# Performance work log

Hardware: AMD Instinct MI355X
Metric: run time of the kernel (lower is better)

## Reference

```python
import jax, jax.numpy as jnp
import numpy as np

B, S, D, H = 4, 1024, 768, 12
DH = D // H            # 64
MAXPOS = 1024          # config.max_position_embeddings
NTYPES = 8             # flow types (embedding has NTYPES+1 rows, row 0 = padding)


def setup_inputs() -> dict:
    key = jax.random.key(0)
    ks = jax.random.split(key, 12)
    sc = 0.02
    inp = {
        "hidden_states": jax.random.normal(ks[0], (B, S, D), jnp.float32),
        "Wq": jax.random.normal(ks[1], (D, D), jnp.float32) * sc,
        "bq": jnp.zeros((D,), jnp.float32),
        "Wk": jax.random.normal(ks[2], (D, D), jnp.float32) * sc,
        "bk": jnp.zeros((D,), jnp.float32),
        "Wv": jax.random.normal(ks[3], (D, D), jnp.float32) * sc,
        "bv": jnp.zeros((D,), jnp.float32),
        "dist_emb": jax.random.normal(ks[4], (2 * MAXPOS - 1, DH), jnp.float32) * sc,
        "cfg_emb": jax.random.normal(ks[5], (NTYPES + 1, 1), jnp.float32) * sc,
        "dfg_emb": jax.random.normal(ks[6], (NTYPES + 1, 1), jnp.float32) * sc,
        "rfg_emb": jax.random.normal(ks[7], (NTYPES + 1, 1), jnp.float32) * sc,
        "cfg_matrix": jax.random.randint(ks[8], (B, S, S), 0, NTYPES + 1, jnp.int32),
        "dfg_matrix": jax.random.randint(ks[9], (B, S, S), 0, NTYPES + 1, jnp.int32),
        "rdg_matrix": jax.random.randint(ks[10], (B, S, S), 0, NTYPES + 1, jnp.int32),
    }
    return inp


def reference(hidden_states, Wq, bq, Wk, bk, Wv, bv, dist_emb,
              cfg_emb, dfg_emb, rfg_emb, cfg_matrix, dfg_matrix, rdg_matrix):
    b, s, d = hidden_states.shape
    inv_sqrt = 1.0 / float(np.sqrt(DH))

    def heads(x):  # [b,s,d] -> [b,H,s,DH]
        return x.reshape(b, s, H, DH).transpose(0, 2, 1, 3)

    q = heads(hidden_states @ Wq.T + bq)
    k = heads(hidden_states @ Wk.T + bk)
    v = heads(hidden_states @ Wv.T + bv)

    scores = jnp.einsum('bhld,bhrd->bhlr', q, k)

    # relative_key_query positional bias
    dist = jnp.arange(s)[:, None] - jnp.arange(s)[None, :] + (MAXPOS - 1)
    pe = dist_emb[dist]  # [s, s, DH]
    scores = scores + jnp.einsum('bhld,lrd->bhlr', q, pe) \
                    + jnp.einsum('bhrd,lrd->bhlr', k, pe)

    scores = scores * inv_sqrt

    # flow-type bias: scalar embedding per (i,j), padding row 0 forced to zero
    flow = (cfg_emb.at[0].set(0.0)[cfg_matrix][..., 0]
            + dfg_emb.at[0].set(0.0)[dfg_matrix][..., 0]
            + rfg_emb.at[0].set(0.0)[rdg_matrix][..., 0])  # [b,s,s]
    scores = scores + flow[:, None, :, :]

    probs = jax.nn.softmax(scores, axis=-1)
    ctx = jnp.einsum('bhlr,bhrd->bhld', probs, v)
    return ctx.transpose(0, 2, 1, 3).reshape(b, s, d)
```

## Files before the change

### kernel.cpp

```cpp
#include <hip/hip_runtime.h>


typedef __attribute__((ext_vector_type(4))) float f32x4;
typedef __attribute__((ext_vector_type(8))) short s16x8;

#define MFMA_BF16 __builtin_amdgcn_mfma_f32_16x16x32_bf16

__device__ __forceinline__ unsigned short f2bf(float x) {
  unsigned u = __builtin_bit_cast(unsigned, x);
  u += 0x7fffu + ((u >> 16) & 1u);
  return (unsigned short)(u >> 16);
}
__device__ __forceinline__ float bf2f(unsigned short h) {
  unsigned u = ((unsigned)h) << 16;
  return __builtin_bit_cast(float, u);
}
__device__ __forceinline__ float exp2_fast(float x) {
  float r;
  asm("v_exp_f32 %0, %1" : "=v"(r) : "v"(x));
  return r;
}
__device__ __forceinline__ void gl_lds16(const void* g, void* l) {
  __builtin_amdgcn_global_load_lds(
      (const __attribute__((address_space(1))) unsigned int*)g,
      (__attribute__((address_space(3))) unsigned int*)l, 16, 0, 0);
}

__global__ __launch_bounds__(256) void k_prep(
    const float* __restrict__ hs, const float* __restrict__ wq,
    const float* __restrict__ wk, const float* __restrict__ wv,
    const float* __restrict__ de, unsigned short* __restrict__ hsb,
    unsigned short* __restrict__ wb, unsigned short* __restrict__ db) {
  const long HSN = 3145728, WN = 1769472;
  long e = ((long)blockIdx.x * 256 + threadIdx.x) * 4;
  if (e < HSN) {
    float4 v = *(const float4*)(hs + e);
    *(ushort4*)(hsb + e) = make_ushort4(f2bf(v.x), f2bf(v.y), f2bf(v.z), f2bf(v.w));
  } else if (e < HSN + WN) {
    long ew = e - HSN;
    const float* src = (ew >= 1179648) ? wv : ((ew >= 589824) ? wk : wq);
    long off = (ew >= 1179648) ? (ew - 1179648) : ((ew >= 589824) ? (ew - 589824) : ew);
    float4 v = *(const float4*)(src + off);
    *(ushort4*)(wb + ew) = make_ushort4(f2bf(v.x), f2bf(v.y), f2bf(v.z), f2bf(v.w));
  } else {
    long ed = e - HSN - WN;
    ushort4 ov;
    if (ed < 131008) {
      float4 v = *(const float4*)(de + ed);
      ov = make_ushort4(f2bf(v.x), f2bf(v.y), f2bf(v.z), f2bf(v.w));
    } else {
      ov = make_ushort4(0, 0, 0, 0);
    }
    *(ushort4*)(db + ed) = ov;
  }
}

__global__ __launch_bounds__(256) void k_flow(
    const int* __restrict__ cm, const int* __restrict__ dm,
    const int* __restrict__ rm, const float* __restrict__ ce,
    const float* __restrict__ dfe, const float* __restrict__ rfe,
    unsigned short* __restrict__ flT) {
  const int tid = threadIdx.x;
  const int rt = blockIdx.x, lt = blockIdx.y, b = blockIdx.z;
  const int l15 = tid & 15, g = (tid >> 4) & 3, w = tid >> 6;
  const int rowb = lt * 64 + w * 16 + g * 4;
  const int colb = rt * 64 + l15;
  s16x8 o0, o1;
#pragma unroll
  for (int n = 0; n < 4; ++n) {
#pragma unroll
    for (int r = 0; r < 4; ++r) {
      const long idx = ((long)b << 20) + ((long)(rowb + r) << 10) + colb + (n << 4);
      const int c = cm[idx], d = dm[idx], rr = rm[idx];
      const float v = (c ? ce[c] : 0.f) + (d ? dfe[d] : 0.f) + (rr ? rfe[rr] : 0.f);
      const short hv = (short)f2bf(1.4426950408889634f * v);
      if (n < 2) o0[n * 4 + r] = hv; else o1[(n - 2) * 4 + r] = hv;
    }
  }
  unsigned short* dst =
      flT + ((long)((((b << 4) + lt) << 4) | rt) << 12) + (tid << 4);
  *(s16x8*)(dst) = o0;
  *(s16x8*)(dst + 8) = o1;
}

__global__ __launch_bounds__(256) void k_qkv(
    const unsigned short* __restrict__ A, const unsigned short* __restrict__ W,
    const float* __restrict__ bq, const float* __restrict__ bk,
    const float* __restrict__ bv, unsigned short* __restrict__ Qp,
    unsigned short* __restrict__ Kp, unsigned short* __restrict__ Vp) {
  __shared__ __align__(16) char smq[16384];
  char* sa = smq;
  char* sb = smq + 8192;
  const int tid = threadIdx.x, w = tid >> 6, lane = tid & 63;
  const int g = lane >> 4, l15 = lane & 15;
  const int n0 = blockIdx.x * 128, m0 = blockIdx.y * 128;
  const int wm = w >> 1, wn = w & 1;
  f32x4 acc[4][4] = {};
  for (int k0 = 0; k0 < 768; k0 += 32) {
#pragma unroll
    for (int it = 0; it < 2; ++it) {
      const int c = (w << 7) + (it << 6) + lane;
      const int row = c >> 2, sl = c & 3;
      const int so = ((sl ^ ((row >> 1) & 3)) << 3);
      char* dst = smq + ((w << 7) + (it << 6)) * 16;
      gl_lds16(A + (long)(m0 + row) * 768 + k0 + so, dst);
      gl_lds16(W + (long)(n0 + row) * 768 + k0 + so, dst + 8192);
    }
    __syncthreads();
    s16x8 af[4], bf[4];
#pragma unroll
    for (int mi = 0; mi < 4; ++mi) {
      const int row = wm * 64 + mi * 16 + l15;
      af[mi] = *(const s16x8*)(sa + row * 64 + ((g ^ ((row >> 1) & 3)) << 4));
    }
#pragma unroll
    for (int ni = 0; ni < 4; ++ni) {
      const int row = wn * 64 + ni * 16 + l15;
      bf[ni] = *(const s16x8*)(sb + row * 64 + ((g ^ ((row >> 1) & 3)) << 4));
    }
#pragma unroll
    for (int mi = 0; mi < 4; ++mi)
#pragma unroll
      for (int ni = 0; ni < 4; ++ni)
        acc[mi][ni] = MFMA_BF16(af[mi], bf[ni], acc[mi][ni], 0, 0, 0);
    __syncthreads();
  }
  const int t_sel = n0 / 768;
  const float* bias = (t_sel == 0) ? bq : (t_sel == 1) ? bk : bv;
  unsigned short* dst = (t_sel == 0) ? Qp : (t_sel == 1) ? Kp : Vp;
#pragma unroll
  for (int ni = 0; ni < 4; ++ni) {
    const int mcol = n0 + wn * 64 + ni * 16 + l15;
    const int nw2 = mcol - t_sel * 768;
    const float bvv = bias[nw2];
    const int h = nw2 >> 6, dh = nw2 & 63;
#pragma unroll
    for (int mi = 0; mi < 4; ++mi) {
#pragma unroll
      for (int r = 0; r < 4; ++r) {
        const int token = m0 + wm * 64 + mi * 16 + (g << 2) + r;
        const int b = token >> 10, s = token & 1023;
        const long idx = ((((long)(b * 12 + h)) << 10) + s) * 64 + dh;
        dst[idx] = f2bf(acc[mi][ni][r] + bvv);
      }
    }
  }
}

__global__ __launch_bounds__(256) void k_vt(const unsigned short* __restrict__ Vp,
                                            unsigned short* __restrict__ Vt) {
  __shared__ __align__(16) unsigned short t[64][64];
  const int bh = blockIdx.y, s0 = blockIdx.x * 64;
  const int tid = threadIdx.x;
#pragma unroll
  for (int it = 0; it < 2; ++it) {
    const int c = it * 256 + tid;
    const int row = c >> 3, sl = c & 7;
    const int slot = sl ^ ((row >> 3) & 7);
    s16x8 v = *(const s16x8*)(Vp + (((long)bh << 10) + s0 + row) * 64 + sl * 8);
    *(s16x8*)&t[row][slot * 8] = v;
  }
  __syncthreads();
#pragma unroll
  for (int it = 0; it < 2; ++it) {
    const int c = it * 256 + tid;
    const int d = c >> 3, ss = c & 7;
    const int cg = d >> 3;
    s16x8 vv;
#pragma unroll
    for (int i = 0; i < 8; ++i) {
      const int rr = ss * 8 + i;
      vv[i] = (short)t[rr][((cg ^ ((rr >> 3) & 7)) << 3) + (d & 7)];
    }
    *(s16x8*)(Vt + (((long)bh * 64 + d) << 10) + s0 + ss * 8) = vv;
  }
}

__global__ __launch_bounds__(256, 3) void k_attn(
    const unsigned short* __restrict__ Qp, const unsigned short* __restrict__ Kp,
    const unsigned short* __restrict__ Vtp, const unsigned short* __restrict__ Db,
    const unsigned short* __restrict__ FlT, float* __restrict__ Out) {
  __shared__ __align__(16) char sm[50688];
  char* Kl = sm;
  char* Vl = sm + 8192;
  char* Dl = sm + 16384;
  unsigned short* QDs = (unsigned short*)(sm + 32768);
  char* Pl = sm + 32768;
  unsigned short* KDs = (unsigned short*)(sm + 41984);

  const int tid = threadIdx.x, w = tid >> 6, lane = tid & 63;
  const int g = lane >> 4, l15 = lane & 15;
  const int l0 = blockIdx.x << 6, h = blockIdx.y, b = blockIdx.z;
  const int bh = b * 12 + h;
  const unsigned short* Qb = Qp + ((long)bh << 16);
  const unsigned short* Kb = Kp + ((long)bh << 16);
  const unsigned short* Vb = Vtp + ((long)bh << 16);
  const unsigned short* fTb =
      FlT + ((long)(((b << 4) + blockIdx.x) << 4) << 12) + (tid << 4);

  const int qrow = l0 + (w << 4) + l15;
  const s16x8 qf0 = *(const s16x8*)(Qb + (long)qrow * 64 + g * 8);
  const s16x8 qf1 = *(const s16x8*)(Qb + (long)qrow * 64 + 32 + g * 8);

  f32x4 oacc[4] = {};
  float lpart[4] = {0.f, 0.f, 0.f, 0.f};

  for (int rt = 0; rt < 16; ++rt) {
    const int r0 = rt << 6;
    const int t0 = l0 - r0 + 960;

    const s16x8 fv0 = *(const s16x8*)(fTb + ((long)rt << 12));
    const s16x8 fv1 = *(const s16x8*)(fTb + ((long)rt << 12) + 8);

#pragma unroll
    for (int it = 0; it < 2; ++it) {
      const int c = (w << 7) + (it << 6) + lane;
      const int row = c >> 3, sl = c & 7;
      const int so = ((sl ^ (row & 7)) << 3);
      char* dst = sm + ((w << 7) + (it << 6)) * 16;
      gl_lds16(Kb + (long)(r0 + row) * 64 + so, dst);
      gl_lds16(Vb + (long)row * 1024 + r0 + so, dst + 8192);
    }
    {
      const int nh = (rt == 0) ? 2 : 1;
      for (int hh = 0; hh < nh; ++hh) {
        const int ts = t0 + (hh << 6);
        char* dhalf = Dl + (((ts >> 6) & 1) << 13);
#pragma unroll
        for (int it = 0; it < 2; ++it) {
          const int c = (w << 7) + (it << 6) + lane;
          const int row = c >> 3, sl = c & 7;
          gl_lds16(Db + (long)(ts + row) * 64 + ((sl ^ (row & 7)) << 3),
                   dhalf + ((w << 7) + (it << 6)) * 16);
        }
      }
    }
    __syncthreads();

    {
      const int krow = (w << 4) + l15;
      const s16x8 kf0 = *(const s16x8*)(Kl + krow * 128 + ((g ^ (krow & 7)) << 4));
      const s16x8 kf1 = *(const s16x8*)(Kl + krow * 128 + (((4 + g) ^ (krow & 7)) << 4));
#pragma unroll
      for (int n = 0; n < 8; ++n) {
        const bool doQ = (n >= w) && (n <= w + 4);
        const bool doK = (n >= 3 - w) && (n <= 7 - w);
        if (!(doQ || doK)) continue;
        const int pb = ((((t0 >> 6) + (n >> 2)) & 1) << 6) + ((n & 3) << 4);
        const int trow = pb + l15;
        const s16x8 d0 = *(const s16x8*)(Dl + trow * 128 + ((g ^ (trow & 7)) << 4));
        const s16x8 d1 = *(const s16x8*)(Dl + trow * 128 + (((4 + g) ^ (trow & 7)) << 4));
        f32x4 qa = {}, ka = {};
        if (doQ) {
          qa = MFMA_BF16(qf0, d0, qa, 0, 0, 0);
          qa = MFMA_BF16(qf1, d1, qa, 0, 0, 0);
        }
        if (doK) {
          ka = MFMA_BF16(kf0, d0, ka, 0, 0, 0);
          ka = MFMA_BF16(kf1, d1, ka, 0, 0, 0);
        }
#pragma unroll
        for (int r = 0; r < 4; ++r) {
          const int prow = (w << 4) + (g << 2) + r;
          const int u = (n << 4) + l15;
          if (doQ) {
            const int cq = u - prow;
            if ((unsigned)cq < 64u) QDs[prow * 72 + cq] = f2bf(qa[r]);
          }
          if (doK) {
            const int ck = u + prow - 63;
            if ((unsigned)ck < 64u) KDs[prow * 68 + ck] = f2bf(ka[r]);
          }
        }
      }
    }
    __syncthreads();

    f32x4 sacc[4] = {};
#pragma unroll
    for (int n = 0; n < 4; ++n) {
      const int kr = (n << 4) + l15;
      const s16x8 b0 = *(const s16x8*)(Kl + kr * 128 + ((g ^ (kr & 7)) << 4));
      const s16x8 b1 = *(const s16x8*)(Kl + kr * 128 + (((4 + g) ^ (kr & 7)) << 4));
      sacc[n] = MFMA_BF16(qf0, b0, sacc[n], 0, 0, 0);
      sacc[n] = MFMA_BF16(qf1, b1, sacc[n], 0, 0, 0);
    }
#pragma unroll
    for (int n = 0; n < 4; ++n) {
#pragma unroll
      for (int r = 0; r < 4; ++r) {
        const int ib = (w << 4) + (g << 2) + r;
        const int j = (n << 4) + l15;
        const float qd = bf2f(QDs[ib * 72 + (63 - j)]);
        const float kd = bf2f(KDs[j * 68 + ib]);
        const float fv = bf2f((unsigned short)(
            n < 2 ? fv0[(n << 2) + r] : fv1[((n - 2) << 2) + r]));
        sacc[n][r] = (sacc[n][r] + qd + kd) * 0.18033688f + fv;
      }
    }

#pragma unroll
    for (int r = 0; r < 4; ++r) {
      const float p0 = exp2_fast(sacc[0][r]);
      const float p1 = exp2_fast(sacc[1][r]);
      const float p2 = exp2_fast(sacc[2][r]);
      const float p3 = exp2_fast(sacc[3][r]);
      sacc[0][r] = p0; sacc[1][r] = p1; sacc[2][r] = p2; sacc[3][r] = p3;
      lpart[r] += (p0 + p1) + (p2 + p3);
    }

#pragma unroll
    for (int n = 0; n < 4; ++n) {
#pragma unroll
      for (int r = 0; r < 4; ++r) {
        const int ib = (w << 4) + (g << 2) + r;
        const int j = (n << 4) + l15;
        *(unsigned short*)(Pl + ib * 144 + (((j >> 3) ^ (ib & 7)) << 4) +
                           ((j & 7) << 1)) = f2bf(sacc[n][r]);
      }
    }

#pragma unroll
    for (int k0 = 0; k0 < 2; ++k0) {
      const int prow = (w << 4) + l15;
      const s16x8 pf = *(const s16x8*)(
          Pl + prow * 144 + ((((k0 << 2) + g) ^ (prow & 7)) << 4));
#pragma unroll
      for (int n = 0; n < 4; ++n) {
        const int vrow = (n << 4) + l15;
        const s16x8 vf = *(const s16x8*)(
            Vl + vrow * 128 + ((((k0 << 2) + g) ^ (vrow & 7)) << 4));
        oacc[n] = MFMA_BF16(pf, vf, oacc[n], 0, 0, 0);
      }
    }
    __syncthreads();
  }

  float lsum[4];
#pragma unroll
  for (int r = 0; r < 4; ++r) {
    float s = lpart[r];
#pragma unroll
    for (int dd = 1; dd < 16; dd <<= 1) s += __shfl_xor(s, dd, 64);
    lsum[r] = s;
  }
#pragma unroll
  for (int n = 0; n < 4; ++n) {
#pragma unroll
    for (int r = 0; r < 4; ++r) {
      const int l = l0 + (w << 4) + (g << 2) + r;
      const int d = (n << 4) + l15;
      Out[((long)(b * 1024 + l)) * 768 + h * 64 + d] = oacc[n][r] / lsum[r];
    }
  }
}

extern "C" void kernel_launch(void* const* d_in, const int* in_sizes, int n_in,
                              void* d_out, int out_size, void* d_ws, size_t ws_size,
                              hipStream_t stream) {
  const float* hs = (const float*)d_in[0];
  const float* Wq = (const float*)d_in[1];
  const float* bq = (const float*)d_in[2];
  const float* Wk = (const float*)d_in[3];
  const float* bk = (const float*)d_in[4];
  const float* Wv = (const float*)d_in[5];
  const float* bv = (const float*)d_in[6];
  const float* de = (const float*)d_in[7];
  const float* ce = (const float*)d_in[8];
  const float* dfe = (const float*)d_in[9];
  const float* rfe = (const float*)d_in[10];
  const int* cm = (const int*)d_in[11];
  const int* dm = (const int*)d_in[12];
  const int* rm = (const int*)d_in[13];
  float* out = (float*)d_out;
  char* ws = (char*)d_ws;

  unsigned short* hsb = (unsigned short*)(ws + 0);
  unsigned short* wb  = (unsigned short*)(ws + 6291456);
  unsigned short* db  = (unsigned short*)(ws + 9830400);
  unsigned short* flT = (unsigned short*)(ws + 10092544);
  unsigned short* qp  = (unsigned short*)(ws + 18481152);
  unsigned short* kp  = (unsigned short*)(ws + 24772608);
  unsigned short* vp  = (unsigned short*)(ws + 31064064);
  unsigned short* vt  = (unsigned short*)(ws + 37355520);

  k_prep<<<4928, 256, 0, stream>>>(hs, Wq, Wk, Wv, de, hsb, wb, db);
  k_flow<<<dim3(16, 16, 4), 256, 0, stream>>>(cm, dm, rm, ce, dfe, rfe, flT);
  k_qkv<<<dim3(18, 32), 256, 0, stream>>>(hsb, wb, bq, bk, bv, qp, kp, vp);
  k_vt<<<dim3(16, 48), 256, 0, stream>>>(vp, vt);
  k_attn<<<dim3(16, 12, 4), 256, 0, stream>>>(qp, kp, vt, db, flT, out);
}
```

Baseline: 137.7 us.

## Keep Q-side relative-position bias in registers via ds_bpermute instead of LDS

The Q·dist_emb bias tiles are now computed into a register array of five MFMA accumulators per wave. The diagonal shift is done with lane permutes (ds_bpermute using precomputed source addresses and masks) rather than a round trip through the QDs shared buffer. The K-side bias loop is also made branch-free over its exact five tiles, with bounds checks only on the edge tiles. This removes LDS stores and loads and the bf16 rounding on the Q path, at the cost of more registers and permute instructions.

```diff
diff --git a/kernel.cpp b/kernel.cpp
--- a/kernel.cpp
+++ b/kernel.cpp
@@ -184,9 +184,8 @@
   char* Kl = sm;
   char* Vl = sm + 8192;
   char* Dl = sm + 16384;
-  unsigned short* QDs = (unsigned short*)(sm + 32768);
-  char* Pl = sm + 32768;
-  unsigned short* KDs = (unsigned short*)(sm + 41984);
+  unsigned short* KDs = (unsigned short*)(sm + 32768);
+  char* Pl = sm + 41472;
 
   const int tid = threadIdx.x, w = tid >> 6, lane = tid & 63;
   const int g = lane >> 4, l15 = lane & 15;
@@ -202,6 +201,16 @@
   const s16x8 qf0 = *(const s16x8*)(Qb + (long)qrow * 64 + g * 8);
   const s16x8 qf1 = *(const s16x8*)(Qb + (long)qrow * 64 + 32 + g * 8);
 
+  int srcad[4];
+  bool msk[4];
+#pragma unroll
+  for (int r = 0; r < 4; ++r) {
+    const int bl = ((g << 2) + r - 1) & 15;
+    srcad[r] = (((lane & 48) + ((bl - l15) & 15)) << 2);
+    msk[r] = (l15 <= bl);
+  }
+  const bool g0 = (g == 0);
+
   f32x4 oacc[4] = {};
   float lpart[4] = {0.f, 0.f, 0.f, 0.f};
 
@@ -237,39 +246,42 @@
     }
     __syncthreads();
 
+    f32x4 qa[5];
+#pragma unroll
+    for (int lt = 0; lt < 5; ++lt) {
+      const int nq = w + lt;
+      const int pb = ((((t0 >> 6) + (nq >> 2)) & 1) << 6) + ((nq & 3) << 4);
+      const int trow = pb + l15;
+      const s16x8 d0 = *(const s16x8*)(Dl + trow * 128 + ((g ^ (trow & 7)) << 4));
+      const s16x8 d1 = *(const s16x8*)(Dl + trow * 128 + (((4 + g) ^ (trow & 7)) << 4));
+      f32x4 a = {};
+      a = MFMA_BF16(qf0, d0, a, 0, 0, 0);
+      a = MFMA_BF16(qf1, d1, a, 0, 0, 0);
+      qa[lt] = a;
+    }
+
     {
       const int krow = (w << 4) + l15;
       const s16x8 kf0 = *(const s16x8*)(Kl + krow * 128 + ((g ^ (krow & 7)) << 4));
       const s16x8 kf1 = *(const s16x8*)(Kl + krow * 128 + (((4 + g) ^ (krow & 7)) << 4));
 #pragma unroll
-      for (int n = 0; n < 8; ++n) {
-        const bool doQ = (n >= w) && (n <= w + 4);
-        const bool doK = (n >= 3 - w) && (n <= 7 - w);
-        if (!(doQ || doK)) continue;
-        const int pb = ((((t0 >> 6) + (n >> 2)) & 1) << 6) + ((n & 3) << 4);
+      for (int kt = 0; kt < 5; ++kt) {
+        const int nk = 3 - w + kt;
+        const int pb = ((((t0 >> 6) + (nk >> 2)) & 1) << 6) + ((nk & 3) << 4);
         const int trow = pb + l15;
         const s16x8 d0 = *(const s16x8*)(Dl + trow * 128 + ((g ^ (trow & 7)) << 4));
         const s16x8 d1 = *(const s16x8*)(Dl + trow * 128 + (((4 + g) ^ (trow & 7)) << 4));
-        f32x4 qa = {}, ka = {};
-        if (doQ) {
-          qa = MFMA_BF16(qf0, d0, qa, 0, 0, 0);
-          qa = MFMA_BF16(qf1, d1, qa, 0, 0, 0);
-        }
-        if (doK) {
-          ka = MFMA_BF16(kf0, d0, ka, 0, 0, 0);
-          ka = MFMA_BF16(kf1, d1, ka, 0, 0, 0);
-        }
+        f32x4 ka = {};
+        ka = MFMA_BF16(kf0, d0, ka, 0, 0, 0);
+        ka = MFMA_BF16(kf1, d1, ka, 0, 0, 0);
 #pragma unroll
         for (int r = 0; r < 4; ++r) {
           const int prow = (w << 4) + (g << 2) + r;
-          const int u = (n << 4) + l15;
-          if (doQ) {
-            const int cq = u - prow;
-            if ((unsigned)cq < 64u) QDs[prow * 72 + cq] = f2bf(qa[r]);
-          }
-          if (doK) {
-            const int ck = u + prow - 63;
+          const int ck = (kt << 4) + l15 + (g << 2) + r - 15;
+          if (kt == 0 || kt == 4) {
             if ((unsigned)ck < 64u) KDs[prow * 68 + ck] = f2bf(ka[r]);
+          } else {
+            KDs[prow * 68 + ck] = f2bf(ka[r]);
           }
         }
       }
@@ -291,7 +303,18 @@
       for (int r = 0; r < 4; ++r) {
         const int ib = (w << 4) + (g << 2) + r;
         const int j = (n << 4) + l15;
-        const float qd = bf2f(QDs[ib * 72 + (63 - j)]);
+        float hi, lo;
+        if (r == 0) {
+          hi = g0 ? qa[3 - n][0] : qa[4 - n][0];
+          lo = qa[3 - n][0];
+        } else {
+          hi = qa[4 - n][r];
+          lo = qa[3 - n][r];
+        }
+        const float vsrc = msk[r] ? hi : lo;
+        const float qd = __builtin_bit_cast(
+            float, __builtin_amdgcn_ds_bpermute(
+                       srcad[r], __builtin_bit_cast(int, vsrc)));
         const float kd = bf2f(KDs[j * 68 + ib]);
         const float fv = bf2f((unsigned short)(
             n < 2 ? fv0[(n << 2) + r] : fv1[((n - 2) << 2) + r]));
```

After: 114.6 us. 1.2x faster.
